# Kernel tuning notes

Measured on AMD Instinct MI355X. Metric: run time of the kernel, lower is better.

Reference implementation:

```python
import jax, jax.numpy as jnp
import numpy as np

N_USERS = 100000
N_ITEMS = 50000
N = N_USERS + N_ITEMS
D = 64
N_LAYERS = 3
E = 3000000


def setup_inputs() -> dict:
    key = jax.random.key(0)
    k1, k2, k3, k4, k5 = jax.random.split(key, 5)
    rows = jax.random.randint(k1, (E,), 0, N, dtype=jnp.int32)
    cols = jax.random.randint(k2, (E,), 0, N, dtype=jnp.int32)
    vals = jax.random.uniform(k3, (E,), dtype=jnp.float32)
    user_emb = jax.random.normal(k4, (N_USERS, D), dtype=jnp.float32) * 0.1
    item_emb = jax.random.normal(k5, (N_ITEMS, D), dtype=jnp.float32) * 0.1
    return {"rows": rows, "cols": cols, "vals": vals,
            "user_emb": user_emb, "item_emb": item_emb}


def _spmm(rows, cols, vals, x):
    # sparse (COO) @ dense: out[r] += vals[e] * x[cols[e]]
    msgs = vals[:, None] * x[cols]  # [E, D]
    return jax.ops.segment_sum(msgs, rows, num_segments=N)


def reference(rows, cols, vals, user_emb, item_emb):
    all_emb = jnp.concatenate([user_emb, item_emb], axis=0)  # [N, D]
    acc = all_emb  # running sum over layer outputs (incl. layer 0)
    for _ in range(N_LAYERS):
        all_emb = _spmm(rows, cols, vals, all_emb)
        acc = acc + all_emb
    light_out = acc / (N_LAYERS + 1)  # mean over stacked layer embeddings
    users_final = light_out[:N_USERS]
    items_final = light_out[N_USERS:]
    return users_final, items_final
```

## Files before the change

### kernel.cpp

```cpp
#include <hip/hip_runtime.h>
#include <hip/hip_fp16.h>

#define N_USERS 100000
#define N_ITEMS 50000
#define N_TOT   150000
#define DIM     64
#define E_EDGES 3000000
#define NP1     (N_TOT + 1)
#define NB1     586
#define EPB     4096
#define SEDGE_MAX 4100000


__global__ void init_kernel(const float* __restrict__ user_emb,
                            const float* __restrict__ item_emb,
                            __half2* __restrict__ b0) {
    int i = blockIdx.x * blockDim.x + threadIdx.x;
    const int total4 = N_TOT * DIM / 4;
    if (i < total4) {
        int base = i * 4;
        float4 v = (base < N_USERS * DIM)
                     ? reinterpret_cast<const float4*>(user_emb)[i]
                     : reinterpret_cast<const float4*>(item_emb)[(base - N_USERS * DIM) >> 2];
        b0[i * 2]     = __floats2half2_rn(v.x, v.y);
        b0[i * 2 + 1] = __floats2half2_rn(v.z, v.w);
    }
}

__global__ void zero_int_kernel(int* __restrict__ p, int n) {
    int i = blockIdx.x * blockDim.x + threadIdx.x;
    if (i < n) p[i] = 0;
}


__global__ __launch_bounds__(256) void hist1_kernel(const int* __restrict__ rows,
                                                    int* __restrict__ hist1) {
    __shared__ int h[NB1];
    for (int b = threadIdx.x; b < NB1; b += 256) h[b] = 0;
    __syncthreads();
    int e0 = blockIdx.x * EPB;
    int cnt = min(EPB, E_EDGES - e0);
    for (int i = threadIdx.x; i < cnt; i += 256)
        atomicAdd(&h[rows[e0 + i] >> 8], 1);
    __syncthreads();
    for (int b = threadIdx.x; b < NB1; b += 256)
        if (h[b]) atomicAdd(&hist1[b], h[b]);
}

__global__ __launch_bounds__(256) void scan586_kernel(const int* __restrict__ src,
                                                      int* __restrict__ dst) {
    __shared__ int psum[256];
    int t = threadIdx.x;
    int i0 = t * 3;
    int s0 = (i0     < NB1) ? src[i0]     : 0;
    int s1 = (i0 + 1 < NB1) ? src[i0 + 1] : 0;
    int s2 = (i0 + 2 < NB1) ? src[i0 + 2] : 0;
    int tsum = s0 + s1 + s2;
    psum[t] = tsum;
    __syncthreads();
    for (int off = 1; off < 256; off <<= 1) {
        int x = (t >= off) ? psum[t - off] : 0;
        __syncthreads();
        psum[t] += x;
        __syncthreads();
    }
    int excl = psum[t] - tsum;
    if (i0     < NB1) dst[i0]     = excl;
    if (i0 + 1 < NB1) dst[i0 + 1] = excl + s0;
    if (i0 + 2 < NB1) dst[i0 + 2] = excl + s0 + s1;
    if (t == 255) dst[NB1] = psum[255];
}

__global__ __launch_bounds__(256) void bin_kernel(const int* __restrict__ rows,
                                                  const int* __restrict__ cols,
                                                  const float* __restrict__ vals,
                                                  const int* __restrict__ bstart,
                                                  int* __restrict__ fill1,
                                                  int2* __restrict__ tmp) {
    __shared__ int sw0[EPB];
    __shared__ int sw1[EPB];
    __shared__ unsigned short sbkt[EPB];
    __shared__ int hist[NB1];
    __shared__ int sstart[NB1];
    __shared__ int gbase[NB1];
    __shared__ int cursor[NB1];
    __shared__ int psum[256];

    int e0 = blockIdx.x * EPB;
    int cnt = min(EPB, E_EDGES - e0);

    for (int b = threadIdx.x; b < NB1; b += 256) hist[b] = 0;
    __syncthreads();

    int r[16], c[16]; float v[16];
#pragma unroll
    for (int k = 0; k < 16; ++k) {
        int i = threadIdx.x + k * 256;
        r[k] = -1;
        if (i < cnt) {
            int e = e0 + i;
            r[k] = rows[e];
            c[k] = cols[e];
            v[k] = vals[e];
            atomicAdd(&hist[r[k] >> 8], 1);
        }
    }
    __syncthreads();

    int t = threadIdx.x;
    int i0 = t * 3;
    int s0 = (i0     < NB1) ? hist[i0]     : 0;
    int s1 = (i0 + 1 < NB1) ? hist[i0 + 1] : 0;
    int s2 = (i0 + 2 < NB1) ? hist[i0 + 2] : 0;
    int tsum = s0 + s1 + s2;
    psum[t] = tsum;
    __syncthreads();
    for (int off = 1; off < 256; off <<= 1) {
        int x = (t >= off) ? psum[t - off] : 0;
        __syncthreads();
        psum[t] += x;
        __syncthreads();
    }
    int excl = psum[t] - tsum;
    if (i0     < NB1) sstart[i0]     = excl;
    if (i0 + 1 < NB1) sstart[i0 + 1] = excl + s0;
    if (i0 + 2 < NB1) sstart[i0 + 2] = excl + s0 + s1;
    __syncthreads();

    for (int b = threadIdx.x; b < NB1; b += 256) {
        int h = hist[b];
        gbase[b] = (h > 0) ? (bstart[b] + atomicAdd(&fill1[b], h)) : 0;
        cursor[b] = sstart[b];
    }
    __syncthreads();

#pragma unroll
    for (int k = 0; k < 16; ++k) {
        if (r[k] >= 0) {
            int b = r[k] >> 8;
            int p = atomicAdd(&cursor[b], 1);
            sw0[p] = ((r[k] & 0xFF) << 24) | c[k];
            sw1[p] = __float_as_int(v[k]);
            sbkt[p] = (unsigned short)b;
        }
    }
    __syncthreads();

    for (int i = threadIdx.x; i < cnt; i += 256) {
        int b = sbkt[i];
        int dest = gbase[b] + (i - sstart[b]);
        tmp[dest] = make_int2(sw0[i], sw1[i]);
    }
}

__global__ __launch_bounds__(256) void bukhist_kernel(const int2* __restrict__ tmp,
                                                      const int* __restrict__ bstart,
                                                      int* __restrict__ rowdeg,
                                                      int* __restrict__ bktpad) {
    int b = blockIdx.x;
    int beg = bstart[b], end = bstart[b + 1];
    __shared__ int hist[256];
    __shared__ int sp[256];
    int t = threadIdx.x;
    hist[t] = 0;
    __syncthreads();
    for (int i = beg + t; i < end; i += 256)
        atomicAdd(&hist[((unsigned)tmp[i].x) >> 24], 1);
    __syncthreads();
    int d = hist[t];
    int r = b * 256 + t;
    if (r < N_TOT) rowdeg[r] = d;
    sp[t] = (d + 7) & ~7;
    __syncthreads();
    for (int off = 128; off > 0; off >>= 1) {
        if (t < off) sp[t] += sp[t + off];
        __syncthreads();
    }
    if (t == 0) bktpad[b] = sp[0];
}

__global__ __launch_bounds__(256) void fsort_kernel(const int* __restrict__ rowdeg,
                                                    const int* __restrict__ pbstart,
                                                    const int* __restrict__ bstart,
                                                    const int2* __restrict__ tmp,
                                                    int* __restrict__ row_ptr,
                                                    int* __restrict__ scol,
                                                    __half* __restrict__ sval) {
    int b = blockIdx.x, t = threadIdx.x;
    int r = b * 256 + t;
    int d = (r < N_TOT) ? rowdeg[r] : 0;
    int pd = (d + 7) & ~7;
    __shared__ int scn[256];
    __shared__ int cursor[256];
    scn[t] = pd;
    __syncthreads();
    for (int off = 1; off < 256; off <<= 1) {
        int x = (t >= off) ? scn[t - off] : 0;
        __syncthreads();
        scn[t] += x;
        __syncthreads();
    }
    int excl = scn[t] - pd;
    int rp = pbstart[b] + excl;
    if (r <= N_TOT) row_ptr[r] = rp;
    cursor[t] = rp;
    if (r < N_TOT) {
        for (int i = d; i < pd; ++i) {
            scol[rp + i] = 0;
            sval[rp + i] = __float2half_rn(0.0f);
        }
    }
    __syncthreads();
    int beg = bstart[b], end = bstart[b + 1];
    for (int i = beg + t; i < end; i += 256) {
        int2 rec = tmp[i];
        int lr = ((unsigned)rec.x) >> 24;
        int p = atomicAdd(&cursor[lr], 1);
        scol[p] = rec.x & 0xFFFFFF;
        sval[p] = __float2half_rn(__int_as_float(rec.y));
    }
}


__global__ __launch_bounds__(256) void spmm2_kernel(const int* __restrict__ row_ptr,
                                                    const int* __restrict__ scol,
                                                    const __half* __restrict__ sval,
                                                    const __half2* __restrict__ src,
                                                    __half2* __restrict__ dst,
                                                    const __half2* __restrict__ c0,
                                                    const __half2* __restrict__ c1,
                                                    float* __restrict__ acc,
                                                    int last) {
    int wid2 = (blockIdx.x * blockDim.x + threadIdx.x) >> 6;
    int lane = threadIdx.x & 63;
    int sub = lane & 31;
    int row = wid2 * 2 + (lane >> 5);
    if (row >= N_TOT) return;
    int beg = row_ptr[row];
    int ng  = (row_ptr[row + 1] - beg) >> 3;
    const int4* cp = reinterpret_cast<const int4*>(scol + beg);
    const int4* vp = reinterpret_cast<const int4*>(sval + beg);
    float s0 = 0.0f, s1 = 0.0f;
    const __half2 z2 = __floats2half2_rn(0.0f, 0.0f);

    if (ng & 1) {
        int4 ci0 = cp[0], ci1 = cp[1];
        int4 vi  = vp[0];
        cp += 2; vp += 1;
        __half2 x0 = src[(unsigned)ci0.x * 32u + sub];
        __half2 x1 = src[(unsigned)ci0.y * 32u + sub];
        __half2 x2 = src[(unsigned)ci0.z * 32u + sub];
        __half2 x3 = src[(unsigned)ci0.w * 32u + sub];
        __half2 x4 = src[(unsigned)ci1.x * 32u + sub];
        __half2 x5 = src[(unsigned)ci1.y * 32u + sub];
        __half2 x6 = src[(unsigned)ci1.z * 32u + sub];
        __half2 x7 = src[(unsigned)ci1.w * 32u + sub];
        const __half2* hv = reinterpret_cast<const __half2*>(&vi);
        __half2 a0 = z2, a1 = z2;
        a0 = __hfma2(__low2half2(hv[0]),  x0, a0);
        a1 = __hfma2(__high2half2(hv[0]), x1, a1);
        a0 = __hfma2(__low2half2(hv[1]),  x2, a0);
        a1 = __hfma2(__high2half2(hv[1]), x3, a1);
        a0 = __hfma2(__low2half2(hv[2]),  x4, a0);
        a1 = __hfma2(__high2half2(hv[2]), x5, a1);
        a0 = __hfma2(__low2half2(hv[3]),  x6, a0);
        a1 = __hfma2(__high2half2(hv[3]), x7, a1);
        float2 fa = __half22float2(__hadd2(a0, a1));
        s0 += fa.x; s1 += fa.y;
    }
    int npair = ng >> 1;
    for (int it = 0; it < npair; ++it) {
        int4 ca = cp[0], cb = cp[1], cc = cp[2], cd = cp[3];
        int4 va = vp[0], vb = vp[1];
        cp += 4; vp += 2;
        __half2 x0  = src[(unsigned)ca.x * 32u + sub];
        __half2 x1  = src[(unsigned)ca.y * 32u + sub];
        __half2 x2  = src[(unsigned)ca.z * 32u + sub];
        __half2 x3  = src[(unsigned)ca.w * 32u + sub];
        __half2 x4  = src[(unsigned)cb.x * 32u + sub];
        __half2 x5  = src[(unsigned)cb.y * 32u + sub];
        __half2 x6  = src[(unsigned)cb.z * 32u + sub];
        __half2 x7  = src[(unsigned)cb.w * 32u + sub];
        __half2 x8  = src[(unsigned)cc.x * 32u + sub];
        __half2 x9  = src[(unsigned)cc.y * 32u + sub];
        __half2 x10 = src[(unsigned)cc.z * 32u + sub];
        __half2 x11 = src[(unsigned)cc.w * 32u + sub];
        __half2 x12 = src[(unsigned)cd.x * 32u + sub];
        __half2 x13 = src[(unsigned)cd.y * 32u + sub];
        __half2 x14 = src[(unsigned)cd.z * 32u + sub];
        __half2 x15 = src[(unsigned)cd.w * 32u + sub];
        const __half2* hva = reinterpret_cast<const __half2*>(&va);
        const __half2* hvb = reinterpret_cast<const __half2*>(&vb);
        __half2 a0 = z2, a1 = z2, a2 = z2, a3 = z2;
        a0 = __hfma2(__low2half2(hva[0]),  x0,  a0);
        a1 = __hfma2(__high2half2(hva[0]), x1,  a1);
        a0 = __hfma2(__low2half2(hva[1]),  x2,  a0);
        a1 = __hfma2(__high2half2(hva[1]), x3,  a1);
        a0 = __hfma2(__low2half2(hva[2]),  x4,  a0);
        a1 = __hfma2(__high2half2(hva[2]), x5,  a1);
        a0 = __hfma2(__low2half2(hva[3]),  x6,  a0);
        a1 = __hfma2(__high2half2(hva[3]), x7,  a1);
        a2 = __hfma2(__low2half2(hvb[0]),  x8,  a2);
        a3 = __hfma2(__high2half2(hvb[0]), x9,  a3);
        a2 = __hfma2(__low2half2(hvb[1]),  x10, a2);
        a3 = __hfma2(__high2half2(hvb[1]), x11, a3);
        a2 = __hfma2(__low2half2(hvb[2]),  x12, a2);
        a3 = __hfma2(__high2half2(hvb[2]), x13, a3);
        a2 = __hfma2(__low2half2(hvb[3]),  x14, a2);
        a3 = __hfma2(__high2half2(hvb[3]), x15, a3);
        float2 f01 = __half22float2(__hadd2(a0, a1));
        float2 f23 = __half22float2(__hadd2(a2, a3));
        s0 += f01.x + f23.x;
        s1 += f01.y + f23.y;
    }
    unsigned o = (unsigned)row * 32u + sub;
    if (last) {
        float2 f0 = __half22float2(c0[o]);
        float2 f1 = __half22float2(c1[o]);
        float2 f2 = __half22float2(src[o]);
        float2 rr;
        rr.x = (f0.x + f1.x + f2.x + s0) * 0.25f;
        rr.y = (f0.y + f1.y + f2.y + s1) * 0.25f;
        reinterpret_cast<float2*>(acc)[o] = rr;
    } else {
        dst[o] = __floats2half2_rn(s0, s1);
    }
}


__global__ void initf_kernel(const float* __restrict__ user_emb,
                             const float* __restrict__ item_emb,
                             float* __restrict__ cur,
                             float* __restrict__ acc) {
    int i = blockIdx.x * blockDim.x + threadIdx.x;
    const int total = N_TOT * DIM;
    if (i < total) {
        float v = (i < N_USERS * DIM) ? user_emb[i] : item_emb[i - N_USERS * DIM];
        cur[i] = v;
        acc[i] = v;
    }
}

__global__ void zero_f_kernel(float* __restrict__ p, int n) {
    int i = blockIdx.x * blockDim.x + threadIdx.x;
    if (i < n) p[i] = 0.0f;
}

__global__ void spmm_atomic_kernel(const int* __restrict__ rows, const int* __restrict__ cols,
                                   const float* __restrict__ vals,
                                   const float* __restrict__ cur, float* __restrict__ next) {
    int tid = blockIdx.x * blockDim.x + threadIdx.x;
    int e = tid >> 4;
    int q = (tid & 15) << 2;
    if (e < E_EDGES) {
        int r = rows[e];
        int c = cols[e];
        float v = vals[e];
        const float4 x = *reinterpret_cast<const float4*>(cur + (size_t)c * DIM + q);
        float* dstp = next + (size_t)r * DIM + q;
        atomicAdd(dstp + 0, v * x.x);
        atomicAdd(dstp + 1, v * x.y);
        atomicAdd(dstp + 2, v * x.z);
        atomicAdd(dstp + 3, v * x.w);
    }
}

__global__ void accum_kernel(float* __restrict__ acc, const float* __restrict__ next, int n) {
    int i = blockIdx.x * blockDim.x + threadIdx.x;
    if (i < n) acc[i] += next[i];
}

__global__ void scale_kernel(float* __restrict__ acc, int n) {
    int i = blockIdx.x * blockDim.x + threadIdx.x;
    if (i < n) acc[i] *= 0.25f;
}


extern "C" void kernel_launch(void* const* d_in, const int* in_sizes, int n_in,
                              void* d_out, int out_size, void* d_ws, size_t ws_size,
                              hipStream_t stream) {
    const int*   rows     = (const int*)d_in[0];
    const int*   cols     = (const int*)d_in[1];
    const float* vals     = (const float*)d_in[2];
    const float* user_emb = (const float*)d_in[3];
    const float* item_emb = (const float*)d_in[4];
    float* acc = (float*)d_out;

    const int total  = N_TOT * DIM;
    const int total2 = total / 2;
    const int tb = 256;

    __half2* b0 = (__half2*)d_ws;
    __half2* b1 = b0 + (size_t)total2;
    __half2* b2 = b1 + (size_t)total2;
    int2* tmp   = (int2*)d_ws;
    int*    scol = (int*)(b2 + (size_t)total2);
    __half* sval = (__half*)(scol + (size_t)SEDGE_MAX);
    int* row_ptr = (int*)(sval + (size_t)SEDGE_MAX);
    int* rowdeg  = row_ptr + NP1;
    int* hist1   = rowdeg + N_TOT;
    int* fill1   = hist1 + NB1;
    int* bktpad  = fill1 + NB1;
    int* bstart  = bktpad + NB1;
    int* pbstart = bstart + NB1 + 1;
    size_t need = (size_t)((char*)(pbstart + NB1 + 1) - (char*)d_ws);

    const int grid_bin = (E_EDGES + EPB - 1) / EPB;

    if (ws_size >= need) {
        zero_int_kernel<<<(2 * NB1 + tb - 1) / tb, tb, 0, stream>>>(hist1, 2 * NB1);
        hist1_kernel<<<grid_bin, tb, 0, stream>>>(rows, hist1);
        scan586_kernel<<<1, tb, 0, stream>>>(hist1, bstart);
        bin_kernel<<<grid_bin, tb, 0, stream>>>(rows, cols, vals, bstart, fill1, tmp);
        bukhist_kernel<<<NB1, tb, 0, stream>>>(tmp, bstart, rowdeg, bktpad);
        scan586_kernel<<<1, tb, 0, stream>>>(bktpad, pbstart);
        fsort_kernel<<<NB1, tb, 0, stream>>>(rowdeg, pbstart, bstart, tmp,
                                             row_ptr, scol, sval);

        dim3 blkInit((total / 4 + tb - 1) / tb);
        init_kernel<<<blkInit, tb, 0, stream>>>(user_emb, item_emb, b0);

        const int waves = N_TOT / 2;
        dim3 blkRows((waves * 64 + tb - 1) / tb);
        spmm2_kernel<<<blkRows, tb, 0, stream>>>(row_ptr, scol, sval, b0, b1, b0, b0, acc, 0);
        spmm2_kernel<<<blkRows, tb, 0, stream>>>(row_ptr, scol, sval, b1, b2, b0, b0, acc, 0);
        spmm2_kernel<<<blkRows, tb, 0, stream>>>(row_ptr, scol, sval, b2, b2, b0, b1, acc, 1);
    } else {
        float* fcur = (float*)d_ws;
        float* fnxt = fcur + (size_t)total;
        dim3 blkTotal((total + tb - 1) / tb);
        initf_kernel<<<blkTotal, tb, 0, stream>>>(user_emb, item_emb, fcur, acc);
        const long long spmm_threads = (long long)E_EDGES * 16;
        dim3 blkSpmm((unsigned)((spmm_threads + tb - 1) / tb));
        for (int layer = 0; layer < 3; ++layer) {
            zero_f_kernel<<<blkTotal, tb, 0, stream>>>(fnxt, total);
            spmm_atomic_kernel<<<blkSpmm, tb, 0, stream>>>(rows, cols, vals, fcur, fnxt);
            accum_kernel<<<blkTotal, tb, 0, stream>>>(acc, fnxt, total);
            float* t = fcur; fcur = fnxt; fnxt = t;
        }
        scale_kernel<<<blkTotal, tb, 0, stream>>>(acc, total);
    }
}
```

Before: 309.1 us.

## Fuse bucket histogram into sort, pack row_ptr with degree, use nontemporal loads/stores

Merges the bucket-histogram, second scan and final sort kernels into one fsort2 kernel that claims its output range with a global atomic cursor, removing two launches and a pass over the temporary edge buffer. The temporary edge records are split into an int column array and a half-precision value array, so the intermediate traffic shrinks. row_ptr now packs the offset and the padded group count into one word, so SpMM reads a single entry per row. SpMM streams edge data with nontemporal loads and writes outputs with nontemporal stores to keep the gathered embedding rows in cache. Buckets now land in nondeterministic order, and the packed row_ptr assumes offsets below 2^24 and fewer than 256 groups per row.

```diff
diff --git a/kernel.cpp b/kernel.cpp
--- a/kernel.cpp
+++ b/kernel.cpp
@@ -10,6 +10,13 @@
 #define NB1     586
 #define EPB     4096
 #define SEDGE_MAX 4100000
+
+typedef int   vi4 __attribute__((ext_vector_type(4)));
+typedef float vf2 __attribute__((ext_vector_type(2)));
+
+__device__ __forceinline__ vi4 nt_load4(const int* p) {
+    return __builtin_nontemporal_load(reinterpret_cast<const vi4*>(p));
+}
 
 
 __global__ void init_kernel(const float* __restrict__ user_emb,
@@ -76,9 +83,10 @@
                                                   const float* __restrict__ vals,
                                                   const int* __restrict__ bstart,
                                                   int* __restrict__ fill1,
-                                                  int2* __restrict__ tmp) {
+                                                  int* __restrict__ tcol,
+                                                  __half* __restrict__ tval) {
     __shared__ int sw0[EPB];
-    __shared__ int sw1[EPB];
+    __shared__ __half swv[EPB];
     __shared__ unsigned short sbkt[EPB];
     __shared__ int hist[NB1];
     __shared__ int sstart[NB1];
@@ -140,7 +148,7 @@
             int b = r[k] >> 8;
             int p = atomicAdd(&cursor[b], 1);
             sw0[p] = ((r[k] & 0xFF) << 24) | c[k];
-            sw1[p] = __float_as_int(v[k]);
+            swv[p] = __float2half_rn(v[k]);
             sbkt[p] = (unsigned short)b;
         }
     }
@@ -149,49 +157,31 @@
     for (int i = threadIdx.x; i < cnt; i += 256) {
         int b = sbkt[i];
         int dest = gbase[b] + (i - sstart[b]);
-        tmp[dest] = make_int2(sw0[i], sw1[i]);
-    }
-}
-
-__global__ __launch_bounds__(256) void bukhist_kernel(const int2* __restrict__ tmp,
-                                                      const int* __restrict__ bstart,
-                                                      int* __restrict__ rowdeg,
-                                                      int* __restrict__ bktpad) {
-    int b = blockIdx.x;
+        tcol[dest] = sw0[i];
+        tval[dest] = swv[i];
+    }
+}
+
+__global__ __launch_bounds__(256) void fsort2_kernel(const int* __restrict__ bstart,
+                                                     const int* __restrict__ tcol,
+                                                     const __half* __restrict__ tval,
+                                                     int* __restrict__ g_cursor,
+                                                     unsigned* __restrict__ row_ptr,
+                                                     int* __restrict__ scol,
+                                                     __half* __restrict__ sval) {
+    int b = blockIdx.x, t = threadIdx.x;
     int beg = bstart[b], end = bstart[b + 1];
     __shared__ int hist[256];
-    __shared__ int sp[256];
-    int t = threadIdx.x;
-    hist[t] = 0;
-    __syncthreads();
-    for (int i = beg + t; i < end; i += 256)
-        atomicAdd(&hist[((unsigned)tmp[i].x) >> 24], 1);
-    __syncthreads();
-    int d = hist[t];
-    int r = b * 256 + t;
-    if (r < N_TOT) rowdeg[r] = d;
-    sp[t] = (d + 7) & ~7;
-    __syncthreads();
-    for (int off = 128; off > 0; off >>= 1) {
-        if (t < off) sp[t] += sp[t + off];
-        __syncthreads();
-    }
-    if (t == 0) bktpad[b] = sp[0];
-}
-
-__global__ __launch_bounds__(256) void fsort_kernel(const int* __restrict__ rowdeg,
-                                                    const int* __restrict__ pbstart,
-                                                    const int* __restrict__ bstart,
-                                                    const int2* __restrict__ tmp,
-                                                    int* __restrict__ row_ptr,
-                                                    int* __restrict__ scol,
-                                                    __half* __restrict__ sval) {
-    int b = blockIdx.x, t = threadIdx.x;
-    int r = b * 256 + t;
-    int d = (r < N_TOT) ? rowdeg[r] : 0;
-    int pd = (d + 7) & ~7;
     __shared__ int scn[256];
     __shared__ int cursor[256];
+    __shared__ int base;
+    hist[t] = 0;
+    __syncthreads();
+    for (int i = beg + t; i < end; i += 256)
+        atomicAdd(&hist[((unsigned)tcol[i]) >> 24], 1);
+    __syncthreads();
+    int d = hist[t];
+    int pd = (d + 7) & ~7;
     scn[t] = pd;
     __syncthreads();
     for (int off = 1; off < 256; off <<= 1) {
@@ -201,28 +191,29 @@
         __syncthreads();
     }
     int excl = scn[t] - pd;
-    int rp = pbstart[b] + excl;
-    if (r <= N_TOT) row_ptr[r] = rp;
+    if (t == 255) base = atomicAdd(g_cursor, scn[255]);
+    __syncthreads();
+    int rp = base + excl;
+    int r = b * 256 + t;
+    if (r < N_TOT) row_ptr[r] = (unsigned)rp | ((unsigned)(pd >> 3) << 24);
     cursor[t] = rp;
+    const __half hz = __float2half_rn(0.0f);
     if (r < N_TOT) {
-        for (int i = d; i < pd; ++i) {
-            scol[rp + i] = 0;
-            sval[rp + i] = __float2half_rn(0.0f);
-        }
-    }
-    __syncthreads();
-    int beg = bstart[b], end = bstart[b + 1];
+        for (int i = d; i < pd; ++i) { scol[rp + i] = 0; sval[rp + i] = hz; }
+    }
+    __syncthreads();
     for (int i = beg + t; i < end; i += 256) {
-        int2 rec = tmp[i];
-        int lr = ((unsigned)rec.x) >> 24;
+        int rec = tcol[i];
+        __half v = tval[i];
+        int lr = ((unsigned)rec) >> 24;
         int p = atomicAdd(&cursor[lr], 1);
-        scol[p] = rec.x & 0xFFFFFF;
-        sval[p] = __float2half_rn(__int_as_float(rec.y));
-    }
-}
-
-
-__global__ __launch_bounds__(256) void spmm2_kernel(const int* __restrict__ row_ptr,
+        scol[p] = rec & 0xFFFFFF;
+        sval[p] = v;
+    }
+}
+
+
+__global__ __launch_bounds__(256) void spmm2_kernel(const unsigned* __restrict__ row_ptr,
                                                     const int* __restrict__ scol,
                                                     const __half* __restrict__ sval,
                                                     const __half2* __restrict__ src,
@@ -236,17 +227,19 @@
     int sub = lane & 31;
     int row = wid2 * 2 + (lane >> 5);
     if (row >= N_TOT) return;
-    int beg = row_ptr[row];
-    int ng  = (row_ptr[row + 1] - beg) >> 3;
-    const int4* cp = reinterpret_cast<const int4*>(scol + beg);
-    const int4* vp = reinterpret_cast<const int4*>(sval + beg);
+    unsigned rp = row_ptr[row];
+    int beg = (int)(rp & 0xFFFFFFu);
+    int ng  = (int)(rp >> 24);
+    const int* cp = scol + beg;
+    const int* vp = reinterpret_cast<const int*>(sval + beg);
     float s0 = 0.0f, s1 = 0.0f;
     const __half2 z2 = __floats2half2_rn(0.0f, 0.0f);
 
     if (ng & 1) {
-        int4 ci0 = cp[0], ci1 = cp[1];
-        int4 vi  = vp[0];
-        cp += 2; vp += 1;
+        vi4 ci0 = nt_load4(cp);
+        vi4 ci1 = nt_load4(cp + 4);
+        vi4 vi  = nt_load4(vp);
+        cp += 8; vp += 4;
         __half2 x0 = src[(unsigned)ci0.x * 32u + sub];
         __half2 x1 = src[(unsigned)ci0.y * 32u + sub];
         __half2 x2 = src[(unsigned)ci0.z * 32u + sub];
@@ -270,9 +263,13 @@
     }
     int npair = ng >> 1;
     for (int it = 0; it < npair; ++it) {
-        int4 ca = cp[0], cb = cp[1], cc = cp[2], cd = cp[3];
-        int4 va = vp[0], vb = vp[1];
-        cp += 4; vp += 2;
+        vi4 ca = nt_load4(cp);
+        vi4 cb = nt_load4(cp + 4);
+        vi4 cc = nt_load4(cp + 8);
+        vi4 cd = nt_load4(cp + 12);
+        vi4 va = nt_load4(vp);
+        vi4 vb = nt_load4(vp + 4);
+        cp += 16; vp += 8;
         __half2 x0  = src[(unsigned)ca.x * 32u + sub];
         __half2 x1  = src[(unsigned)ca.y * 32u + sub];
         __half2 x2  = src[(unsigned)ca.z * 32u + sub];
@@ -318,12 +315,15 @@
         float2 f0 = __half22float2(c0[o]);
         float2 f1 = __half22float2(c1[o]);
         float2 f2 = __half22float2(src[o]);
-        float2 rr;
+        vf2 rr;
         rr.x = (f0.x + f1.x + f2.x + s0) * 0.25f;
         rr.y = (f0.y + f1.y + f2.y + s1) * 0.25f;
-        reinterpret_cast<float2*>(acc)[o] = rr;
+        __builtin_nontemporal_store(rr, reinterpret_cast<vf2*>(acc) + o);
     } else {
-        dst[o] = __floats2half2_rn(s0, s1);
+        __half2 hres = __floats2half2_rn(s0, s1);
+        int ires;
+        __builtin_memcpy(&ires, &hres, 4);
+        __builtin_nontemporal_store(ires, reinterpret_cast<int*>(dst) + o);
     }
 }
 
@@ -393,29 +393,26 @@
     __half2* b0 = (__half2*)d_ws;
     __half2* b1 = b0 + (size_t)total2;
     __half2* b2 = b1 + (size_t)total2;
-    int2* tmp   = (int2*)d_ws;
+    int*    tcol = (int*)d_ws;
+    __half* tval = (__half*)b1;
     int*    scol = (int*)(b2 + (size_t)total2);
     __half* sval = (__half*)(scol + (size_t)SEDGE_MAX);
-    int* row_ptr = (int*)(sval + (size_t)SEDGE_MAX);
-    int* rowdeg  = row_ptr + NP1;
-    int* hist1   = rowdeg + N_TOT;
+    unsigned* row_ptr = (unsigned*)(sval + (size_t)SEDGE_MAX);
+    int* hist1   = (int*)(row_ptr + NP1);
     int* fill1   = hist1 + NB1;
-    int* bktpad  = fill1 + NB1;
-    int* bstart  = bktpad + NB1;
-    int* pbstart = bstart + NB1 + 1;
-    size_t need = (size_t)((char*)(pbstart + NB1 + 1) - (char*)d_ws);
+    int* g_cur   = fill1 + NB1;
+    int* bstart  = g_cur + 1;
+    size_t need = (size_t)((char*)(bstart + NB1 + 1) - (char*)d_ws);
 
     const int grid_bin = (E_EDGES + EPB - 1) / EPB;
 
     if (ws_size >= need) {
-        zero_int_kernel<<<(2 * NB1 + tb - 1) / tb, tb, 0, stream>>>(hist1, 2 * NB1);
+        zero_int_kernel<<<(2 * NB1 + 1 + tb - 1) / tb, tb, 0, stream>>>(hist1, 2 * NB1 + 1);
         hist1_kernel<<<grid_bin, tb, 0, stream>>>(rows, hist1);
         scan586_kernel<<<1, tb, 0, stream>>>(hist1, bstart);
-        bin_kernel<<<grid_bin, tb, 0, stream>>>(rows, cols, vals, bstart, fill1, tmp);
-        bukhist_kernel<<<NB1, tb, 0, stream>>>(tmp, bstart, rowdeg, bktpad);
-        scan586_kernel<<<1, tb, 0, stream>>>(bktpad, pbstart);
-        fsort_kernel<<<NB1, tb, 0, stream>>>(rowdeg, pbstart, bstart, tmp,
-                                             row_ptr, scol, sval);
+        bin_kernel<<<grid_bin, tb, 0, stream>>>(rows, cols, vals, bstart, fill1, tcol, tval);
+        fsort2_kernel<<<NB1, tb, 0, stream>>>(bstart, tcol, tval, g_cur,
+                                              row_ptr, scol, sval);
 
         dim3 blkInit((total / 4 + tb - 1) / tb);
         init_kernel<<<blkInit, tb, 0, stream>>>(user_emb, item_emb, b0);
```

Result: slower. 327.5 us (+6.0%).
